# Kernel optimization log

Hardware: AMD Instinct MI355X
Metric: run time of the kernel (lower is better)

## Reference

```python
import jax, jax.numpy as jnp
import numpy as np

B, T, D, H, C = 64, 512, 128, 512, 256  # batch, seq_len, input_dim, rnn_dim, clf hidden


def _lstm_cell(x, h, c, Wih, Whh, b):
    # PyTorch gate order: i, f, g, o; b = bias_ih + bias_hh
    gates = x @ Wih.T + h @ Whh.T + b  # [B, 4H]
    i, f, g, o = jnp.split(gates, 4, axis=-1)
    c = jax.nn.sigmoid(f) * c + jax.nn.sigmoid(i) * jnp.tanh(g)
    h = jax.nn.sigmoid(o) * jnp.tanh(c)
    return h, c


def _run_lstm2(xs, state, p0, p1):
    # xs: [B, T, in]; state: (h0, c0, h1, c1) each [B, H]
    def step(carry, x_t):
        h0, c0, h1, c1 = carry
        h0, c0 = _lstm_cell(x_t, h0, c0, *p0)
        h1, c1 = _lstm_cell(h0, h1, c1, *p1)
        return (h0, c0, h1, c1), h1
    state, ys = jax.lax.scan(step, state, jnp.swapaxes(xs, 0, 1))
    return jnp.swapaxes(ys, 0, 1), state


def setup_inputs() -> dict:
    key = jax.random.key(0)
    ks = jax.random.split(key, 18)
    s = 0.04  # ~1/sqrt(H), matches torch LSTM init scale
    w = lambda k, shape: (jax.random.normal(k, shape, jnp.float32) * s)
    inp = {
        "x": jax.random.uniform(ks[0], (B, T, D), dtype=jnp.float32),
        "y": (jax.random.uniform(ks[1], (B, T, D), dtype=jnp.float32) > 0.9).astype(jnp.float32),
        "enc_Wih0": w(ks[2], (4 * H, D)), "enc_Whh0": w(ks[3], (4 * H, H)), "enc_b0": w(ks[4], (4 * H,)),
        "enc_Wih1": w(ks[5], (4 * H, H)), "enc_Whh1": w(ks[6], (4 * H, H)), "enc_b1": w(ks[7], (4 * H,)),
        "dec_Wih0": w(ks[8], (4 * H, D)), "dec_Whh0": w(ks[9], (4 * H, H)), "dec_b0": w(ks[10], (4 * H,)),
        "dec_Wih1": w(ks[11], (4 * H, H)), "dec_Whh1": w(ks[12], (4 * H, H)), "dec_b1": w(ks[13], (4 * H,)),
        "clf_W1": w(ks[14], (C, H)), "clf_b1": w(ks[15], (C,)),
        "clf_W2": w(ks[16], (D, C)), "clf_b2": w(ks[17], (D,)),
    }
    return inp


def reference(x, y, enc_Wih0, enc_Whh0, enc_b0, enc_Wih1, enc_Whh1, enc_b1,
              dec_Wih0, dec_Whh0, dec_b0, dec_Wih1, dec_Whh1, dec_b1,
              clf_W1, clf_b1, clf_W2, clf_b2):
    Bc = x.shape[0]
    z = jnp.zeros((Bc, H), x.dtype)
    # encoder: only final (h, c) of both layers is used
    _, state = _run_lstm2(x, (z, z, z, z),
                          (enc_Wih0, enc_Whh0, enc_b0), (enc_Wih1, enc_Whh1, enc_b1))
    # decoder under full teacher forcing: steps t=1..T-1 consume y[:, t-1]
    dec_out, _ = _run_lstm2(y[:, :-1], state,
                            (dec_Wih0, dec_Whh0, dec_b0), (dec_Wih1, dec_Whh1, dec_b1))
    hid = jax.nn.relu(dec_out @ clf_W1.T + clf_b1)          # [B, T-1, C]
    logits = hid @ clf_W2.T + clf_b2                        # [B, T-1, D]
    # outputs[:, 0] stays zero, as in the torch loop starting at t=1
    return jnp.concatenate([jnp.zeros_like(logits[:, :1]), logits], axis=1)
```

## Files before the change

kernel.cpp:

```cpp
#include <hip/hip_runtime.h>
#include <hip/hip_bf16.h>
#include <stdint.h>

#define SMEM_BYTES 150528

using short8  = __attribute__((ext_vector_type(8))) short;
using f32x4   = __attribute__((ext_vector_type(4))) float;
using u32x4   = __attribute__((ext_vector_type(4))) unsigned int;

#define OXBF 0u
#define OYBF 8388608u
#define OWE0 16777216u
#define OWD0 (OWE0 + 2621440u)
#define OWE1 (OWD0 + 2621440u)
#define OWD1 (OWE1 + 4194304u)
#define OWC1 (OWD1 + 4194304u)
#define OWC2 (OWC1 + 262144u)
#define OA0  (OWC2 + 65536u)
#define OB0  (OA0 + 524288u)
#define OA1  (OB0 + 524288u)
#define OB1  (OA1 + 524288u)
#define OHP  (OB1 + 524288u)
#define OFLG (OHP + 262144u)
#define OFC1 (OFLG + 4096u)
#define OFH  (OFLG + 8192u)
#define OFL  (OFLG + 9216u)
#define OPRB (OFLG + 16384u)
#define OVOT (OFLG + 32768u)

#define GUARD (1<<19)

static __device__ __forceinline__ unsigned short f2bf(float f){
  union { float f; unsigned u; } v; v.f = f;
  unsigned r = v.u + 0x7FFFu + ((v.u >> 16) & 1u);
  return (unsigned short)(r >> 16);
}
static __device__ __forceinline__ float sigm(float x){ return 1.f/(1.f+__expf(-x)); }
static __device__ __forceinline__ float tanh_(float x){ return 1.f - 2.f/(__expf(2.f*x)+1.f); }

static __device__ __forceinline__ u32x4 ld_r16(const void* p, bool loc){
  u32x4 v;
  if (loc) asm volatile("global_load_dwordx4 %0, %1, off sc0"     : "=v"(v) : "v"(p) : "memory");
  else     asm volatile("global_load_dwordx4 %0, %1, off sc0 sc1" : "=v"(v) : "v"(p) : "memory");
  return v;
}
static __device__ __forceinline__ void st_r16(void* p, u32x4 v, bool loc){
  if (loc) asm volatile("global_store_dwordx4 %0, %1, off sc0"     :: "v"(p), "v"(v) : "memory");
  else     asm volatile("global_store_dwordx4 %0, %1, off sc0 sc1" :: "v"(p), "v"(v) : "memory");
}
static __device__ __forceinline__ unsigned ld_f4(const void* p, bool loc){
  unsigned v;
  if (loc) asm volatile("global_load_dword %0, %1, off sc0\n\ts_waitcnt vmcnt(0)"     : "=v"(v) : "v"(p) : "memory");
  else     asm volatile("global_load_dword %0, %1, off sc0 sc1\n\ts_waitcnt vmcnt(0)" : "=v"(v) : "v"(p) : "memory");
  return v;
}
static __device__ __forceinline__ unsigned ld_f4a(const void* p, bool loc){
  unsigned v;
  if (loc) asm volatile("global_load_dword %0, %1, off sc0"     : "=v"(v) : "v"(p) : "memory");
  else     asm volatile("global_load_dword %0, %1, off sc0 sc1" : "=v"(v) : "v"(p) : "memory");
  return v;
}
static __device__ __forceinline__ void st_f4(void* p, unsigned v, bool loc){
  if (loc) asm volatile("global_store_dword %0, %1, off sc0"     :: "v"(p), "v"(v) : "memory");
  else     asm volatile("global_store_dword %0, %1, off sc0 sc1" :: "v"(p), "v"(v) : "memory");
}
static __device__ __forceinline__ void drain_vm(){
  asm volatile("s_waitcnt vmcnt(0)" ::: "memory");
}
static __device__ __forceinline__ bool isS(u32x4 v){
  return (v[0]==0xFFFFFFFFu) | (v[1]==0xFFFFFFFFu) | (v[2]==0xFFFFFFFFu) | (v[3]==0xFFFFFFFFu);
}

__global__ void k_init(float* __restrict__ out, uint8_t* __restrict__ ws){
  int i = blockIdx.x*blockDim.x + threadIdx.x;
  int ns = gridDim.x*blockDim.x;
  uint32_t* r = (uint32_t*)(ws + OA0);
  const int nring = (4*524288 + 262144)/4;
  for (int k=i; k<nring; k+=ns) r[k] = 0xFFFFFFFFu;
  uint32_t* fl = (uint32_t*)(ws + OFLG);
  for (int k=i; k<49152/4; k+=ns) fl[k] = 0u;
  for (int k=i; k<64*128; k+=ns) out[(size_t)(k>>7)*(512*128) + (k&127)] = 0.f;
}

__global__ void k_cvt(const float* __restrict__ x, const float* __restrict__ y,
                      uint8_t* __restrict__ ws){
  unsigned short* xb = (unsigned short*)(ws + OXBF);
  unsigned short* yb = (unsigned short*)(ws + OYBF);
  const int n = 64*512*128;
  int i = blockIdx.x*blockDim.x + threadIdx.x, ns = gridDim.x*blockDim.x;
  for (int k=i; k<n; k+=ns){ xb[k] = f2bf(x[k]); yb[k] = f2bf(y[k]); }
}

__global__ void k_swzgate(const float* __restrict__ Wih, const float* __restrict__ Whh,
                          uint8_t* __restrict__ ws, size_t dstOff, int Kin, int KC, int NKK, int mode){
  unsigned short* dst = (unsigned short*)(ws + dstOff);
  const int total = 2048 * (KC*4);
  int i = blockIdx.x*blockDim.x + threadIdx.x, ns = gridDim.x*blockDim.x;
  for (int idx=i; idx<total; idx+=ns){
    int j = idx & 7;
    int lane = (idx >> 3) & 63;
    int t = idx >> 9;
    int g = t & 3; t >>= 2;
    int kk = t % NKK; t /= NKK;
    int w = t & 3; int ub = t >> 2;
    int off = ((lane>>4)<<3) + j;
    int k = mode ? (kk==0 ? w*32 + off : 128 + w*128 + (kk-1)*32 + off)
                 : (w*KC + kk*32 + off);
    int u = ub*16 + (lane&15);
    int row = g*512 + u;
    float v = (k < Kin) ? Wih[(size_t)row*Kin + k] : Whh[(size_t)row*512 + (k-Kin)];
    dst[idx] = f2bf(v);
  }
}

__global__ void k_swzclf(const float* __restrict__ W, uint8_t* __restrict__ ws,
                         size_t dstOff, int nwgs, int Kw, int Ktot){
  unsigned short* dst = (unsigned short*)(ws + dstOff);
  const int NKK = Kw/32;
  const int total = nwgs*4*NKK*64*8;
  int i = blockIdx.x*blockDim.x + threadIdx.x, ns = gridDim.x*blockDim.x;
  for (int idx=i; idx<total; idx+=ns){
    int j = idx & 7;
    int lane = (idx >> 3) & 63;
    int t = idx >> 9;
    int kk = t % NKK; t /= NKK;
    int w = t & 3; int wg = t >> 2;
    int k = w*Kw + kk*32 + ((lane>>4)<<3) + j;
    int col = wg*16 + (lane&15);
    dst[idx] = f2bf(W[(size_t)col*Ktot + k]);
  }
}

__launch_bounds__(256, 1)
__global__ void k_seq(uint8_t* __restrict__ ws,
                      const float* __restrict__ eb0, const float* __restrict__ eb1,
                      const float* __restrict__ db0, const float* __restrict__ db1,
                      const float* __restrict__ cb1, const float* __restrict__ cb2,
                      float* __restrict__ out){
  __shared__ uint8_t smem[SMEM_BYTES];
  const int wg = blockIdx.x, tid = threadIdx.x;
  const int w = tid>>6, l = tid&63, lr = l&15, lg = l>>4;
  const int xcd = wg & 7, j = wg >> 3;

  int role;
  if (xcd < 2) role = 0;
  else if (xcd < 4) role = 1;
  else if (xcd == 4 && j < 16) role = 2;
  else if (xcd == 4 && j < 24) role = 3;
  else return;

  const unsigned short* xb = (const unsigned short*)(ws+OXBF);
  const unsigned short* yb = (const unsigned short*)(ws+OYBF);
  unsigned short* A0e = (unsigned short*)(ws+OA0);
  unsigned short* B0e = (unsigned short*)(ws+OB0);
  unsigned short* A1e = (unsigned short*)(ws+OA1);
  unsigned short* B1e = (unsigned short*)(ws+OB1);
  unsigned short* hpr = (unsigned short*)(ws+OHP);

  short8* BL = (short8*)smem;
  float*  P0 = (float*)(smem + 131072);
  float*  P1 = (float*)(smem + 139776);
  unsigned short* HS = (unsigned short*)(smem + 148480);

  const u32x4 S4 = (u32x4){0xFFFFFFFFu,0xFFFFFFFFu,0xFFFFFFFFu,0xFFFFFFFFu};
  const u32x4 Z4 = (u32x4){0u,0u,0u,0u};

  bool loc;
  {
    const int n   = (role <= 1) ? 32 : 24;
    const int bas = (role <= 1) ? xcd : 4;
    if (w == 0){
      bool ok = true;
      #pragma unroll 1
      for (int gen = 1; gen <= 3; ++gen){
        if (l == 0) st_f4(ws + OPRB + (size_t)wg*64u, (unsigned)gen, true);
        if (l < n){
          const void* p = ws + OPRB + (size_t)(bas + 8*l)*64u;
          int spins = 0; unsigned e;
          do { e = ld_f4(p, true); } while ((int)e < gen && ++spins < 1024);
          if ((int)e < gen) ok = false;
        }
      }
      unsigned long long b1 = __ballot(ok);
      bool wgok = (b1 == ~0ULL);
      if (l == 0) st_f4(ws + OVOT + (size_t)wg*64u, wgok ? 2u : 1u, false);
      bool vok = wgok;
      if (l < n){
        const void* p = ws + OVOT + (size_t)(bas + 8*l)*64u;
        unsigned v;
        do { v = ld_f4(p, false); } while (v == 0u);
        vok = vok && (v == 2u);
      }
      unsigned long long b2 = __ballot(vok);
      if (l == 0) *(int*)HS = (b2 == ~0ULL) ? 1 : 0;
    }
    __syncthreads();
    loc = (*(volatile int*)HS) != 0;
    __syncthreads();
  }

  auto loadB = [&](size_t srcOff, int bytes){
    const u32x4* s = (const u32x4*)(ws + srcOff);
    u32x4* d = (u32x4*)smem;
    for (int i = tid; i < bytes/16; i += 256) d[i] = s[i];
  };

  if (role <= 1){
    const bool isC0 = (role == 0);
    const int bt = isC0 ? xcd : xcd-2, ub = j;
    const int u = tid&15, ug = ub*16 + u;
    const int bbytes = isC0 ? 81920 : 131072;
    unsigned short* OWN0 = loc ? A0e : B0e;

    float be[4], bd[4];
    {
      const float* e = isC0 ? eb0 : eb1;
      const float* d = isC0 ? db0 : db1;
      #pragma unroll
      for (int g=0; g<4; ++g){ be[g] = e[g*512+ug]; bd[g] = d[g*512+ug]; }
    }
    loadB((isC0 ? (size_t)OWE0 : (size_t)OWE1) + (size_t)ub*bbytes, bbytes);
    float cS0 = 0.f, cS1 = 0.f;
    __syncthreads();

    for (int t = 0; t < 1023; ++t){
      if (t == 512){
        __syncthreads();
        loadB((isC0 ? (size_t)OWD0 : (size_t)OWD1) + (size_t)ub*bbytes, bbytes);
        __syncthreads();
      }

      const int slotW = t&7, slotR = (t+7)&7, slotC = (t+3)&7;

      const bool gateAct = isC0 ? (t >= 4) : (t >= 517);
      const int  ng      = isC0 ? 32 : 16;
      const void* fp = isC0 ? (const void*)(ws + OFC1 + (size_t)(bt*32 + (l&31))*64)
                            : (const void*)(ws + OFH  + (size_t)(l&15)*64);
      unsigned fv = 0u;
      if (w == 0 && l < ng && gateAct) fv = ld_f4a(fp, false);

      f32x4 acc[2][4];
      #pragma unroll
      for (int m=0;m<2;++m)
        #pragma unroll
        for (int g=0;g<4;++g) acc[m][g] = (f32x4){0.f,0.f,0.f,0.f};

      if (isC0){
        const unsigned short* xs = (t<512) ? xb : yb;
        const int tt = (t<512) ? t : t-512;
        short8 ax[2];
        #pragma unroll
        for (int m=0;m<2;++m){
          const int b = bt*32 + m*16 + lr;
          ax[m] = *(const short8*)(xs + ((size_t)b*512 + tt)*128 + w*32 + (lg<<3));
        }
        u32x4 ah[4][2];
        if (t > 0){
          const unsigned short* base = OWN0 + (size_t)slotR*64*512;
          int gd = 0; bool bad;
          do {
            #pragma unroll
            for (int kk=0; kk<4; ++kk)
              #pragma unroll
              for (int m=0;m<2;++m){
                const int b = bt*32 + m*16 + lr;
                ah[kk][m] = ld_r16(base + (size_t)b*512 + w*128 + kk*32 + (lg<<3), loc);
              }
            drain_vm();
            __builtin_amdgcn_sched_barrier(0);
            bad = false;
            #pragma unroll
            for (int kk=0; kk<4; ++kk)
              #pragma unroll
              for (int m=0;m<2;++m) bad |= isS(ah[kk][m]);
            if (bad) __builtin_amdgcn_s_sleep(1);
          } while (bad && ++gd < GUARD);
          __builtin_amdgcn_sched_barrier(0);
        } else {
          #pragma unroll
          for (int kk=0; kk<4; ++kk)
            #pragma unroll
            for (int m=0;m<2;++m) ah[kk][m] = Z4;
        }
        #pragma unroll
        for (int g=0;g<4;++g){
          short8 bf = BL[((w*5+0)*4+g)*64 + l];
          acc[0][g] = __builtin_amdgcn_mfma_f32_16x16x32_bf16(ax[0], bf, acc[0][g],0,0,0);
          acc[1][g] = __builtin_amdgcn_mfma_f32_16x16x32_bf16(ax[1], bf, acc[1][g],0,0,0);
        }
        #pragma unroll
        for (int kk=1; kk<5; ++kk)
          #pragma unroll
          for (int g=0;g<4;++g){
            short8 bf = BL[((w*5+kk)*4+g)*64 + l];
            acc[0][g] = __builtin_amdgcn_mfma_f32_16x16x32_bf16(__builtin_bit_cast(short8, ah[kk-1][0]), bf, acc[0][g],0,0,0);
            acc[1][g] = __builtin_amdgcn_mfma_f32_16x16x32_bf16(__builtin_bit_cast(short8, ah[kk-1][1]), bf, acc[1][g],0,0,0);
          }
      } else {
        u32x4 a[8][2];
        const bool wv01 = (w < 2);
        if (wv01 || t > 0){
          const unsigned short* base;
          bool myloc;
          if (wv01){ base = B0e + (size_t)slotW*64*512; myloc = false; }
          else {
            base = (loc ? A1e : (((t-1) >= 512) ? B1e : A1e)) + (size_t)slotR*64*512;
            myloc = loc;
          }
          const int kbase = wv01 ? (w*256) : (w*256 - 512);
          int gd = 0; bool bad;
          do {
            #pragma unroll
            for (int kk=0; kk<8; ++kk)
              #pragma unroll
              for (int m=0;m<2;++m){
                const int b = bt*32 + m*16 + lr;
                a[kk][m] = ld_r16(base + (size_t)b*512 + kbase + kk*32 + (lg<<3), myloc);
              }
            drain_vm();
            __builtin_amdgcn_sched_barrier(0);
            bad = false;
            #pragma unroll
            for (int kk=0; kk<8; ++kk)
              #pragma unroll
              for (int m=0;m<2;++m) bad |= isS(a[kk][m]);
            if (bad) __builtin_amdgcn_s_sleep(1);
          } while (bad && ++gd < GUARD);
          __builtin_amdgcn_sched_barrier(0);
        } else {
          #pragma unroll
          for (int kk=0; kk<8; ++kk)
            #pragma unroll
            for (int m=0;m<2;++m) a[kk][m] = Z4;
        }
        #pragma unroll
        for (int kk=0; kk<8; ++kk)
          #pragma unroll
          for (int g=0;g<4;++g){
            short8 bf = BL[((w*8+kk)*4+g)*64 + l];
            acc[0][g] = __builtin_amdgcn_mfma_f32_16x16x32_bf16(__builtin_bit_cast(short8, a[kk][0]), bf, acc[0][g],0,0,0);
            acc[1][g] = __builtin_amdgcn_mfma_f32_16x16x32_bf16(__builtin_bit_cast(short8, a[kk][1]), bf, acc[1][g],0,0,0);
          }
      }

      {
        float* P = (w&1) ? P1 : P0;
        if (w < 2){
          #pragma unroll
          for (int m=0;m<2;++m)
            #pragma unroll
            for (int g=0;g<4;++g)
              #pragma unroll
              for (int r=0;r<4;++r)
                P[(m*16 + (lg<<2) + r)*68 + g*16 + lr] = acc[m][g][r];
        }
        __syncthreads();
        if (w >= 2){
          #pragma unroll
          for (int m=0;m<2;++m)
            #pragma unroll
            for (int g=0;g<4;++g)
              #pragma unroll
              for (int r=0;r<4;++r)
                P[(m*16 + (lg<<2) + r)*68 + g*16 + lr] += acc[m][g][r];
        }
        __syncthreads();
      }

      if (w == 0){
        drain_vm();
        __builtin_amdgcn_sched_barrier(0);
        if (gateAct && l < ng){
          const int n0 = isC0 ? (t-4) : (t-516);
          const int need = (n0 < 1) ? 1 : n0;
          int v = (int)fv, gd = 0;
          while (v < need && ++gd < GUARD){ v = (int)ld_f4(fp, false); __builtin_amdgcn_s_sleep(2); }
        }
        if (t >= 4 && t <= 1019){
          const int row = l>>1, half = l&1;
          const size_t off = ((size_t)slotC*64 + bt*32 + row)*512 + ub*16 + half*8;
          if (isC0){
            st_r16(OWN0 + off, S4, loc);
            if (loc) st_r16(B0e + off, S4, false);
          } else {
            if (loc){
              st_r16(A1e + off, S4, true);
              if (t+3 >= 512) st_r16(B1e + off, S4, false);
            } else {
              st_r16(((t+3 >= 512) ? B1e : A1e) + off, S4, false);
            }
          }
        }
      }

      const float* bias = (t<512) ? be : bd;
      #pragma unroll
      for (int s=0;s<2;++s){
        const int row = (tid>>4) + s*16;
        const int pi = row*68 + u;
        float gi = P0[pi]      + P1[pi]      + bias[0];
        float gf = P0[pi+16]   + P1[pi+16]   + bias[1];
        float gg = P0[pi+32]   + P1[pi+32]   + bias[2];
        float go = P0[pi+48]   + P1[pi+48]   + bias[3];
        float cprev = s ? cS1 : cS0;
        float c = sigm(gf)*cprev + sigm(gi)*tanh_(gg);
        if (s) cS1 = c; else cS0 = c;
        float h = sigm(go)*tanh_(c);
        HS[row*16 + u] = f2bf(h);
      }
      __syncthreads();
      if (tid < 64){
        u32x4 v = *(const u32x4*)(HS + tid*8);
        const int row = tid>>1, half = tid&1;
        const size_t off = ((size_t)slotW*64 + bt*32 + row)*512 + ub*16 + half*8;
        if (isC0){
          st_r16(OWN0 + off, v, loc);
          if (loc) st_r16(B0e + off, v, false);
        } else {
          if (loc){
            st_r16(A1e + off, v, true);
            if (t >= 512) st_r16(B1e + off, v, false);
          } else {
            st_r16(((t >= 512) ? B1e : A1e) + off, v, false);
          }
        }
      }
      if (!isC0 && tid == 0)
        st_f4(ws + OFC1 + (size_t)(bt*32+ub)*64, (unsigned)(t+1), false);
    }
  } else if (role == 2){
    const int hwg = j;
    const int u = tid&15, col = hwg*16 + u;
    const float bc = cb1[col];
    loadB((size_t)OWC1 + (size_t)hwg*16384, 16384);
    __syncthreads();
    for (int t2 = 0; t2 < 511; ++t2){
      const int slot = t2&7, slotC = (t2+3)&7;
      const bool gateAct = (t2 >= 5);
      const void* fp = (const void*)(ws + OFL + (size_t)(l&7)*64);
      unsigned fv = 0u;
      if (w == 0 && l < 8 && gateAct) fv = ld_f4a(fp, loc);

      u32x4 a[4][4];
      const unsigned short* base = B1e + (size_t)slot*64*512;
      int gd = 0; bool bad;
      do {
        #pragma unroll
        for (int kk=0; kk<4; ++kk)
          #pragma unroll
          for (int m=0;m<4;++m)
            a[kk][m] = ld_r16(base + (size_t)(m*16+lr)*512 + w*128 + kk*32 + (lg<<3), false);
        drain_vm();
        __builtin_amdgcn_sched_barrier(0);
        bad = false;
        #pragma unroll
        for (int kk=0; kk<4; ++kk)
          #pragma unroll
          for (int m=0;m<4;++m) bad |= isS(a[kk][m]);
        if (bad) __builtin_amdgcn_s_sleep(1);
      } while (bad && ++gd < GUARD);
      __builtin_amdgcn_sched_barrier(0);
      f32x4 ha[4];
      #pragma unroll
      for (int m=0;m<4;++m) ha[m] = (f32x4){0.f,0.f,0.f,0.f};
      #pragma unroll
      for (int kk=0; kk<4; ++kk){
        short8 bf = BL[(w*4+kk)*64 + l];
        #pragma unroll
        for (int m=0;m<4;++m)
          ha[m] = __builtin_amdgcn_mfma_f32_16x16x32_bf16(__builtin_bit_cast(short8, a[kk][m]), bf, ha[m],0,0,0);
      }
      {
        float* P = (w&1) ? P1 : P0;
        if (w < 2){
          #pragma unroll
          for (int m=0;m<4;++m)
            #pragma unroll
            for (int r=0;r<4;++r)
              P[(m*16 + (lg<<2) + r)*20 + lr] = ha[m][r];
        }
        __syncthreads();
        if (w >= 2){
          #pragma unroll
          for (int m=0;m<4;++m)
            #pragma unroll
            for (int r=0;r<4;++r)
              P[(m*16 + (lg<<2) + r)*20 + lr] += ha[m][r];
        }
        __syncthreads();
      }
      if (w == 0){
        drain_vm();
        __builtin_amdgcn_sched_barrier(0);
        if (gateAct && l < 8){
          const int n0 = t2 - 4;
          const int need = (n0 < 1) ? 1 : n0;
          int v = (int)fv, g2 = 0;
          while (v < need && ++g2 < GUARD){ v = (int)ld_f4(fp, loc); __builtin_amdgcn_s_sleep(2); }
        }
        if (t2 >= 5 && t2 <= 507){
          #pragma unroll
          for (int q=0;q<2;++q)
            st_r16(hpr + ((size_t)slotC*64 + l)*256 + hwg*16 + q*8, S4, loc);
        }
      }
      #pragma unroll
      for (int s=0;s<4;++s){
        const int row = (tid>>4) + s*16;
        float v = P0[row*20+u] + P1[row*20+u] + bc;
        HS[row*16 + u] = f2bf(fmaxf(v, 0.f));
      }
      __syncthreads();
      if (tid < 128){
        u32x4 v = *(const u32x4*)(HS + tid*8);
        const int row = tid>>1, half = tid&1;
        st_r16(hpr + ((size_t)slot*64 + row)*256 + hwg*16 + half*8, v, loc);
      }
      if (tid == 0) st_f4(ws + OFH + (size_t)hwg*64, (unsigned)(t2+1), false);
    }
  } else {
    const int lwg = j - 16;
    const int u = tid&15, col = lwg*16 + u;
    const float bc = cb2[col];
    loadB((size_t)OWC2 + (size_t)lwg*8192, 8192);
    __syncthreads();
    for (int t3 = 0; t3 < 511; ++t3){
      const int slot = t3&7;
      u32x4 a[2][4];
      const unsigned short* base = hpr + (size_t)slot*64*256;
      int gd = 0; bool bad;
      do {
        #pragma unroll
        for (int kk=0; kk<2; ++kk)
          #pragma unroll
          for (int m=0;m<4;++m)
            a[kk][m] = ld_r16(base + (size_t)(m*16+lr)*256 + w*64 + kk*32 + (lg<<3), loc);
        drain_vm();
        __builtin_amdgcn_sched_barrier(0);
        bad = false;
        #pragma unroll
        for (int kk=0; kk<2; ++kk)
          #pragma unroll
          for (int m=0;m<4;++m) bad |= isS(a[kk][m]);
        if (bad) __builtin_amdgcn_s_sleep(1);
      } while (bad && ++gd < GUARD);
      __builtin_amdgcn_sched_barrier(0);
      f32x4 la[4];
      #pragma unroll
      for (int m=0;m<4;++m) la[m] = (f32x4){0.f,0.f,0.f,0.f};
      #pragma unroll
      for (int kk=0; kk<2; ++kk){
        short8 bf = BL[(w*2+kk)*64 + l];
        #pragma unroll
        for (int m=0;m<4;++m)
          la[m] = __builtin_amdgcn_mfma_f32_16x16x32_bf16(__builtin_bit_cast(short8, a[kk][m]), bf, la[m],0,0,0);
      }
      {
        float* P = (w&1) ? P1 : P0;
        if (w < 2){
          #pragma unroll
          for (int m=0;m<4;++m)
            #pragma unroll
            for (int r=0;r<4;++r)
              P[(m*16 + (lg<<2) + r)*20 + lr] = la[m][r];
        }
        __syncthreads();
        if (w >= 2){
          #pragma unroll
          for (int m=0;m<4;++m)
            #pragma unroll
            for (int r=0;r<4;++r)
              P[(m*16 + (lg<<2) + r)*20 + lr] += la[m][r];
        }
        __syncthreads();
      }
      #pragma unroll
      for (int s=0;s<4;++s){
        const int row = (tid>>4) + s*16;
        float v = P0[row*20+u] + P1[row*20+u] + bc;
        out[((size_t)row*512 + (t3+1))*128 + col] = v;
      }
      if (tid == 0) st_f4(ws + OFL + (size_t)lwg*64, (unsigned)(t3+1), loc);
    }
  }
}

extern "C" void kernel_launch(void* const* d_in, const int* in_sizes, int n_in,
                              void* d_out, int out_size, void* d_ws, size_t ws_size,
                              hipStream_t stream){
  const float* x   = (const float*)d_in[0];
  const float* y   = (const float*)d_in[1];
  const float* eW0 = (const float*)d_in[2];
  const float* eU0 = (const float*)d_in[3];
  const float* eb0 = (const float*)d_in[4];
  const float* eW1 = (const float*)d_in[5];
  const float* eU1 = (const float*)d_in[6];
  const float* eb1 = (const float*)d_in[7];
  const float* dW0 = (const float*)d_in[8];
  const float* dU0 = (const float*)d_in[9];
  const float* db0 = (const float*)d_in[10];
  const float* dW1 = (const float*)d_in[11];
  const float* dU1 = (const float*)d_in[12];
  const float* db1 = (const float*)d_in[13];
  const float* cW1 = (const float*)d_in[14];
  const float* cb1 = (const float*)d_in[15];
  const float* cW2 = (const float*)d_in[16];
  const float* cb2 = (const float*)d_in[17];
  float* out = (float*)d_out;
  uint8_t* ws = (uint8_t*)d_ws;
  (void)in_sizes; (void)n_in; (void)out_size; (void)ws_size;

  k_init<<<dim3(256), dim3(256), 0, stream>>>(out, ws);
  k_cvt<<<dim3(2048), dim3(256), 0, stream>>>(x, y, ws);
  k_swzgate<<<dim3(1280), dim3(256), 0, stream>>>(eW0, eU0, ws, (size_t)OWE0, 128, 160, 5, 1);
  k_swzgate<<<dim3(1280), dim3(256), 0, stream>>>(dW0, dU0, ws, (size_t)OWD0, 128, 160, 5, 1);
  k_swzgate<<<dim3(2048), dim3(256), 0, stream>>>(eW1, eU1, ws, (size_t)OWE1, 512, 256, 8, 0);
  k_swzgate<<<dim3(2048), dim3(256), 0, stream>>>(dW1, dU1, ws, (size_t)OWD1, 512, 256, 8, 0);
  k_swzclf<<<dim3(256), dim3(256), 0, stream>>>(cW1, ws, (size_t)OWC1, 16, 128, 512);
  k_swzclf<<<dim3(64),  dim3(256), 0, stream>>>(cW2, ws, (size_t)OWC2, 8, 64, 256);
  k_seq<<<dim3(256), dim3(256), 0, stream>>>(ws, eb0, eb1, db0, db1, cb1, cb2, out);
}
```

Measured before the change: 5.281 ms.

## Deepen ring buffers to 32 slots and batch slot-clearing and flag waits every 8 steps

Enlarges the inter-workgroup ring buffers from 8 to 32 slots and replaces per-step consumer-progress checks and sentinel refills with a check every 8 steps that refills 8 slots at once. This is meant to take the per-step flag polling and sentinel stores off the critical recurrent path. The cost is more workspace memory, bursty stores every 8 steps, and a more complex slot-index scheme. The role-2 slot mapping (512+t2)&31 also has to stay consistent with the producers.

```diff
diff --git a/kernel.cpp b/kernel.cpp
--- a/kernel.cpp
+++ b/kernel.cpp
@@ -17,11 +17,11 @@
 #define OWC1 (OWD1 + 4194304u)
 #define OWC2 (OWC1 + 262144u)
 #define OA0  (OWC2 + 65536u)
-#define OB0  (OA0 + 524288u)
-#define OA1  (OB0 + 524288u)
-#define OB1  (OA1 + 524288u)
-#define OHP  (OB1 + 524288u)
-#define OFLG (OHP + 262144u)
+#define OB0  (OA0 + 2097152u)
+#define OA1  (OB0 + 2097152u)
+#define OB1  (OA1 + 2097152u)
+#define OHP  (OB1 + 2097152u)
+#define OFLG (OHP + 1048576u)
 #define OFC1 (OFLG + 4096u)
 #define OFH  (OFLG + 8192u)
 #define OFL  (OFLG + 9216u)
@@ -54,16 +54,12 @@
   else     asm volatile("global_load_dword %0, %1, off sc0 sc1\n\ts_waitcnt vmcnt(0)" : "=v"(v) : "v"(p) : "memory");
   return v;
 }
-static __device__ __forceinline__ unsigned ld_f4a(const void* p, bool loc){
-  unsigned v;
-  if (loc) asm volatile("global_load_dword %0, %1, off sc0"     : "=v"(v) : "v"(p) : "memory");
-  else     asm volatile("global_load_dword %0, %1, off sc0 sc1" : "=v"(v) : "v"(p) : "memory");
-  return v;
-}
 static __device__ __forceinline__ void st_f4(void* p, unsigned v, bool loc){
   if (loc) asm volatile("global_store_dword %0, %1, off sc0"     :: "v"(p), "v"(v) : "memory");
   else     asm volatile("global_store_dword %0, %1, off sc0 sc1" :: "v"(p), "v"(v) : "memory");
 }
+static __device__ __forceinline__ unsigned ld_cg4(const void* p){ return ld_f4(p, false); }
+static __device__ __forceinline__ void st_cg4(void* p, unsigned v){ st_f4(p, v, false); }
 static __device__ __forceinline__ void drain_vm(){
   asm volatile("s_waitcnt vmcnt(0)" ::: "memory");
 }
@@ -75,7 +71,7 @@
   int i = blockIdx.x*blockDim.x + threadIdx.x;
   int ns = gridDim.x*blockDim.x;
   uint32_t* r = (uint32_t*)(ws + OA0);
-  const int nring = (4*524288 + 262144)/4;
+  const int nring = (4*2097152 + 1048576)/4;
   for (int k=i; k<nring; k+=ns) r[k] = 0xFFFFFFFFu;
   uint32_t* fl = (uint32_t*)(ws + OFLG);
   for (int k=i; k<49152/4; k+=ns) fl[k] = 0u;
@@ -230,14 +226,7 @@
         __syncthreads();
       }
 
-      const int slotW = t&7, slotR = (t+7)&7, slotC = (t+3)&7;
-
-      const bool gateAct = isC0 ? (t >= 4) : (t >= 517);
-      const int  ng      = isC0 ? 32 : 16;
-      const void* fp = isC0 ? (const void*)(ws + OFC1 + (size_t)(bt*32 + (l&31))*64)
-                            : (const void*)(ws + OFH  + (size_t)(l&15)*64);
-      unsigned fv = 0u;
-      if (w == 0 && l < ng && gateAct) fv = ld_f4a(fp, false);
+      const int slotW = t&31, slotR = (t+31)&31;
 
       f32x4 acc[2][4];
       #pragma unroll
@@ -367,27 +356,38 @@
         __syncthreads();
       }
 
-      if (w == 0){
+      if (w == 0 && (t & 7) == 0){
         drain_vm();
         __builtin_amdgcn_sched_barrier(0);
-        if (gateAct && l < ng){
-          const int n0 = isC0 ? (t-4) : (t-516);
-          const int need = (n0 < 1) ? 1 : n0;
-          int v = (int)fv, gd = 0;
-          while (v < need && ++gd < GUARD){ v = (int)ld_f4(fp, false); __builtin_amdgcn_s_sleep(2); }
-        }
-        if (t >= 4 && t <= 1019){
+        if (isC0){
+          if (t >= 24 && l < 32){
+            const void* p = ws + OFC1 + (size_t)(bt*32+l)*64;
+            const int need = (t-22 < 1) ? 1 : t-22;
+            int v, gd = 0;
+            do { v = (int)ld_f4(p, false); if (v < need) __builtin_amdgcn_s_sleep(2); }
+            while (v < need && ++gd < GUARD);
+          }
+        } else {
+          if (t >= 536 && l < 16){
+            const void* p = ws + OFH + (size_t)l*64;
+            const int need = (t-534 < 1) ? 1 : t-534;
+            int v, gd = 0;
+            do { v = (int)ld_f4(p, false); if (v < need) __builtin_amdgcn_s_sleep(2); }
+            while (v < need && ++gd < GUARD);
+          }
+        }
+        if (t >= 8){
           const int row = l>>1, half = l&1;
-          const size_t off = ((size_t)slotC*64 + bt*32 + row)*512 + ub*16 + half*8;
-          if (isC0){
-            st_r16(OWN0 + off, S4, loc);
-            if (loc) st_r16(B0e + off, S4, false);
-          } else {
-            if (loc){
-              st_r16(A1e + off, S4, true);
-              if (t+3 >= 512) st_r16(B1e + off, S4, false);
+          #pragma unroll
+          for (int a=2; a<=9; ++a){
+            const int cs = (t+a)&31;
+            const size_t off = ((size_t)cs*64 + bt*32 + row)*512 + ub*16 + half*8;
+            if (isC0){
+              st_r16(OWN0 + off, S4, loc);
+              if (loc) st_r16(B0e + off, S4, false);
             } else {
-              st_r16(((t+3 >= 512) ? B1e : A1e) + off, S4, false);
+              st_r16(loc ? A1e + off : (((t+a-32) >= 512) ? B1e + off : A1e + off), S4, loc ? true : false);
+              if (loc && (t+a) >= 544) st_r16(B1e + off, S4, false);
             }
           }
         }
@@ -435,11 +435,7 @@
     loadB((size_t)OWC1 + (size_t)hwg*16384, 16384);
     __syncthreads();
     for (int t2 = 0; t2 < 511; ++t2){
-      const int slot = t2&7, slotC = (t2+3)&7;
-      const bool gateAct = (t2 >= 5);
-      const void* fp = (const void*)(ws + OFL + (size_t)(l&7)*64);
-      unsigned fv = 0u;
-      if (w == 0 && l < 8 && gateAct) fv = ld_f4a(fp, loc);
+      const int slot = (512+t2)&31;
 
       u32x4 a[4][4];
       const unsigned short* base = B1e + (size_t)slot*64*512;
@@ -489,19 +485,24 @@
         }
         __syncthreads();
       }
-      if (w == 0){
+      if (w == 0 && (t2 & 7) == 0){
         drain_vm();
         __builtin_amdgcn_sched_barrier(0);
-        if (gateAct && l < 8){
-          const int n0 = t2 - 4;
-          const int need = (n0 < 1) ? 1 : n0;
-          int v = (int)fv, g2 = 0;
-          while (v < need && ++g2 < GUARD){ v = (int)ld_f4(fp, loc); __builtin_amdgcn_s_sleep(2); }
-        }
-        if (t2 >= 5 && t2 <= 507){
-          #pragma unroll
-          for (int q=0;q<2;++q)
-            st_r16(hpr + ((size_t)slotC*64 + l)*256 + hwg*16 + q*8, S4, loc);
+        if (t2 >= 24 && l < 8){
+          const void* p = ws + OFL + (size_t)l*64;
+          const int need = (t2-22 < 1) ? 1 : t2-22;
+          int v, g2 = 0;
+          do { v = (int)ld_f4(p, loc); if (v < need) __builtin_amdgcn_s_sleep(2); }
+          while (v < need && ++g2 < GUARD);
+        }
+        if (t2 >= 8){
+          #pragma unroll
+          for (int a=2; a<=9; ++a){
+            const int cs = (t2+a)&31;
+            #pragma unroll
+            for (int q=0;q<2;++q)
+              st_r16(hpr + ((size_t)cs*64 + l)*256 + hwg*16 + q*8, S4, loc);
+          }
         }
       }
       #pragma unroll
@@ -514,7 +515,7 @@
       if (tid < 128){
         u32x4 v = *(const u32x4*)(HS + tid*8);
         const int row = tid>>1, half = tid&1;
-        st_r16(hpr + ((size_t)slot*64 + row)*256 + hwg*16 + half*8, v, loc);
+        st_r16(hpr + ((size_t)(t2&31)*64 + row)*256 + hwg*16 + half*8, v, loc);
       }
       if (tid == 0) st_f4(ws + OFH + (size_t)hwg*64, (unsigned)(t2+1), false);
     }
@@ -525,7 +526,7 @@
     loadB((size_t)OWC2 + (size_t)lwg*8192, 8192);
     __syncthreads();
     for (int t3 = 0; t3 < 511; ++t3){
-      const int slot = t3&7;
+      const int slot = t3&31;
       u32x4 a[2][4];
       const unsigned short* base = hpr + (size_t)slot*64*256;
       int gd = 0; bool bad;
```

After: 5.209 ms. About the same (-1.4%).
